# Optimization experiments

Measured on AMD Instinct MI355X. Metric: run time of the kernel, lower is better.

The kernel has to match this reference:

```python
import jax, jax.numpy as jnp
import numpy as np

B_, T_, D_MODEL = 2, 2048, 1024
EXPAND, D_STATE, D_CONV, HEADDIM = 2, 128, 4, 64
D_INNER = EXPAND * D_MODEL            # 2048
NHEADS = D_INNER // HEADDIM           # 32
CONV_DIM = D_INNER + 2 * D_STATE      # 2304 (x, B, C share the depthwise conv)
D_IN_PROJ = 2 * D_INNER + 2 * D_STATE + NHEADS  # z, xBC, dt


def _rmsnorm(x, w, eps=1e-5):
    return x * jax.lax.rsqrt(jnp.mean(x * x, axis=-1, keepdims=True) + eps) * w


def setup_inputs() -> dict:
    key = jax.random.key(0)
    ks = jax.random.split(key, 8)
    def s(k, shape, scale=0.02):
        return jax.random.normal(k, shape, jnp.float32) * scale
    x = jax.random.normal(ks[0], (B_, T_, D_MODEL), jnp.float32)
    W_in = s(ks[1], (D_MODEL, D_IN_PROJ))
    conv_w = s(ks[2], (CONV_DIM, D_CONV), 0.1)
    conv_b = jnp.zeros((CONV_DIM,), jnp.float32)
    # dt_bias = softplus^-1(dt_init) with dt in [1e-3, 1e-1], per Mamba init
    dt0 = jax.random.uniform(ks[3], (NHEADS,), minval=1e-3, maxval=1e-1)
    dt_bias = jnp.log(jnp.expm1(dt0))
    A_log = jnp.log(jax.random.uniform(ks[4], (NHEADS,), minval=1.0, maxval=16.0))
    D = jnp.ones((NHEADS,), jnp.float32)
    norm_w = jnp.ones((D_MODEL,), jnp.float32)
    gnorm_w = jnp.ones((D_INNER,), jnp.float32)
    W_out = s(ks[5], (D_INNER, D_MODEL))
    return {"x": x, "W_in": W_in, "conv_w": conv_w, "conv_b": conv_b,
            "dt_bias": dt_bias, "A_log": A_log, "D": D,
            "norm_w": norm_w, "gnorm_w": gnorm_w, "W_out": W_out}


def reference(x, W_in, conv_w, conv_b, dt_bias, A_log, D, norm_w, gnorm_w, W_out):
    res = x
    xn = _rmsnorm(x, norm_w)                       # pre-norm
    zxbcdt = xn @ W_in                             # (B,T,D_IN_PROJ)
    z = zxbcdt[..., :D_INNER]
    xBC = zxbcdt[..., D_INNER:D_INNER + CONV_DIM]
    dt = zxbcdt[..., D_INNER + CONV_DIM:]          # (B,T,H)
    # causal depthwise conv over time on concat(x,B,C)
    inp = jnp.transpose(xBC, (0, 2, 1))            # (B,C,T)
    kern = conv_w[:, None, :]                      # (C,1,K)
    conv = jax.lax.conv_general_dilated(
        inp, kern, window_strides=(1,), padding=[(D_CONV - 1, 0)],
        feature_group_count=CONV_DIM, dimension_numbers=("NCH", "OIH", "NCH"))
    xBC = jax.nn.silu(jnp.transpose(conv, (0, 2, 1)) + conv_b)
    xs = xBC[..., :D_INNER].reshape(B_, T_, NHEADS, HEADDIM)  # (B,T,H,P)
    Bm = xBC[..., D_INNER:D_INNER + D_STATE]       # (B,T,N), ngroups=1
    C = xBC[..., D_INNER + D_STATE:]               # (B,T,N)
    dt = jax.nn.softplus(dt + dt_bias)             # (B,T,H)
    A = -jnp.exp(A_log)                            # (H,)

    def step(h, inps):
        x_t, B_t, C_t, dt_t = inps                 # (B,H,P),(B,N),(B,N),(B,H)
        da = jnp.exp(dt_t * A)                     # (B,H)
        h = h * da[:, :, None, None] + (dt_t[..., None] * x_t)[..., None] * B_t[:, None, None, :]
        y = jnp.einsum("bhpn,bn->bhp", h, C_t) + D[None, :, None] * x_t
        return h, y

    h0 = jnp.zeros((B_, NHEADS, HEADDIM, D_STATE), x.dtype)
    seq = (jnp.moveaxis(xs, 1, 0), jnp.moveaxis(Bm, 1, 0),
           jnp.moveaxis(C, 1, 0), jnp.moveaxis(dt, 1, 0))
    _, ys = jax.lax.scan(step, h0, seq)            # ys: (T,B,H,P)
    y = jnp.moveaxis(ys, 0, 1).reshape(B_, T_, D_INNER)
    y = _rmsnorm(y * jax.nn.silu(z), gnorm_w)      # gated RMSNorm
    return y @ W_out + res
```

## Files before the change

kernel.cpp:

```cpp
#include <hip/hip_runtime.h>
#include <hip/hip_bf16.h>

typedef unsigned short u16;
typedef unsigned int u32;
typedef u16 u16x8 __attribute__((ext_vector_type(8)));
typedef __bf16 bf16x8 __attribute__((ext_vector_type(8)));
typedef float f32x4 __attribute__((ext_vector_type(4)));

#define B_SZ 2
#define T_SZ 2048
#define DMODEL 1024
#define DINNER 2048
#define DSTATE 128
#define NHEADS 32
#define HEADDIM 64
#define CONVDIM 2304
#define DINPROJ 4384
#define DINPROJ_P 4480
#define NROWS (B_SZ * T_SZ)
#define L_CH 128
#define NCH 16

__device__ __forceinline__ float bf2f(u16 u) {
    union { float f; u32 i; } v; v.i = ((u32)u) << 16; return v.f;
}
__device__ __forceinline__ u16 f2bf(float f) {
    union { float f; u32 i; } v; v.f = f;
    u32 r = v.i + 0x7FFFu + ((v.i >> 16) & 1u);
    return (u16)(r >> 16);
}
__device__ __forceinline__ bf16x8 ldfrag(const u16* p) {
    return __builtin_bit_cast(bf16x8, *(const u16x8*)p);
}
__device__ __forceinline__ void gload_lds16(const u16* g, u16* l) {
    __builtin_amdgcn_global_load_lds(
        (const __attribute__((address_space(1))) unsigned int*)g,
        (__attribute__((address_space(3))) unsigned int*)l, 16, 0, 0);
}

__device__ void trans_tile(const float* __restrict__ in, u16* __restrict__ out,
                           int K, int N, int n0, int k0)
{
    __shared__ u16 tile[64][66];
    const int tid = threadIdx.x;
#pragma unroll
    for (int r = 0; r < 16; r++) {
        int idx = r * 256 + tid;
        int k = idx >> 6, n = idx & 63;
        float v = (n0 + n < N) ? in[(size_t)(k0 + k) * N + n0 + n] : 0.f;
        tile[n][k] = f2bf(v);
    }
    __syncthreads();
#pragma unroll
    for (int r = 0; r < 16; r++) {
        int idx = r * 256 + tid;
        int n = idx >> 6, k = idx & 63;
        out[(size_t)(n0 + n) * K + k0 + k] = tile[n][k];
    }
}

__global__ __launch_bounds__(256) void prep_kernel(
    const float* __restrict__ W_in, u16* __restrict__ W_inT,
    const float* __restrict__ W_out, u16* __restrict__ W_outT,
    const float* __restrict__ x, const float* __restrict__ nw, u16* __restrict__ xn,
    const float* __restrict__ cw, u16* __restrict__ cwT)
{
    const int blk = blockIdx.x;
    const int tid = threadIdx.x;
    if (blk < 1120) {
        trans_tile(W_in, W_inT, DMODEL, DINPROJ, (blk % 70) * 64, (blk / 70) * 64);
    } else if (blk < 1632) {
        int idx = blk - 1120;
        trans_tile(W_out, W_outT, DINNER, DMODEL, (idx % 16) * 64, (idx / 16) * 64);
    } else if (blk < 5728) {
        const int row = blk - 1632;
        const float* xr = x + (size_t)row * DMODEL;
        float vals[4]; float ss = 0.f;
#pragma unroll
        for (int i = 0; i < 4; i++) {
            int c = tid + i * 256;
            float v = xr[c]; vals[i] = v; ss += v * v;
        }
#pragma unroll
        for (int o = 32; o; o >>= 1) ss += __shfl_xor(ss, o);
        __shared__ float red[4];
        if ((tid & 63) == 0) red[tid >> 6] = ss;
        __syncthreads();
        ss = red[0] + red[1] + red[2] + red[3];
        float sc = rsqrtf(ss / (float)DMODEL + 1e-5f);
#pragma unroll
        for (int i = 0; i < 4; i++) {
            int c = tid + i * 256;
            xn[(size_t)row * DMODEL + c] = f2bf(vals[i] * sc * nw[c]);
        }
    } else {
        for (int idx = tid; idx < 4 * CONVDIM; idx += 256) {
            int k = idx / CONVDIM, c = idx - k * CONVDIM;
            cwT[idx] = f2bf(cw[c * 4 + k]);
        }
    }
}

template<int MODE, int KC>
__global__ __launch_bounds__(256) void gemm128_kernel(
    const u16* __restrict__ A, const u16* __restrict__ BT, void* __restrict__ Cv,
    const float* __restrict__ Res, int Nst, int nbx)
{
    __shared__ u16 As[128 * 64];
    __shared__ u16 Bs[128 * 64];
    const int tid = threadIdx.x;
    const int l = tid & 63, w = tid >> 6;
    const int per = nbx * 8;
    const int grp = blockIdx.x / per, r = blockIdx.x % per;
    const int m0 = (grp * 8 + (r & 7)) * 128;
    const int n0 = (r >> 3) * 128;
    const int ml = l & 15, quad = l >> 4;
    const int wm = (w & 1) * 64, wn = (w >> 1) * 64;
    f32x4 acc[4][4] = {};
    const int srow = l >> 3;
    const int sgx = (l & 7) ^ srow;
    const u16* Ag = A + (size_t)(m0 + w * 8 + srow) * KC + sgx * 8;
    const u16* Bg = BT + (size_t)(n0 + w * 8 + srow) * KC + sgx * 8;
    u16* const As_w = &As[(w * 8) * 64];
    u16* const Bs_w = &Bs[(w * 8) * 64];

#pragma unroll 4
    for (int k0 = 0; k0 < KC; k0 += 64) {
        __syncthreads();
#pragma unroll
        for (int j = 0; j < 4; j++) {
            gload_lds16(Ag + (size_t)(j * 32) * KC + k0, As_w + j * 32 * 64);
            gload_lds16(Bg + (size_t)(j * 32) * KC + k0, Bs_w + j * 32 * 64);
        }
        __syncthreads();
#pragma unroll
        for (int ks4 = 0; ks4 < 2; ks4++) {
            bf16x8 af[4], bfr[4];
#pragma unroll
            for (int i = 0; i < 4; i++)
                af[i] = ldfrag(&As[(wm + i * 16 + ml) * 64 +
                                   (((ks4 * 4 + quad) ^ (ml & 7)) * 8)]);
#pragma unroll
            for (int i = 0; i < 4; i++)
                bfr[i] = ldfrag(&Bs[(wn + i * 16 + ml) * 64 +
                                    (((ks4 * 4 + quad) ^ (ml & 7)) * 8)]);
#pragma unroll
            for (int mt = 0; mt < 4; mt++)
#pragma unroll
                for (int nt = 0; nt < 4; nt++)
                    acc[mt][nt] = __builtin_amdgcn_mfma_f32_16x16x32_bf16(
                        af[mt], bfr[nt], acc[mt][nt], 0, 0, 0);
        }
    }
#pragma unroll
    for (int mt = 0; mt < 4; mt++)
#pragma unroll
        for (int nt = 0; nt < 4; nt++)
#pragma unroll
            for (int rg = 0; rg < 4; rg++) {
                int m = m0 + wm + mt * 16 + quad * 4 + rg;
                int n = n0 + wn + nt * 16 + ml;
                if (n < Nst) {
                    if (MODE == 0)
                        ((u16*)Cv)[(size_t)m * Nst + n] = f2bf(acc[mt][nt][rg]);
                    else
                        ((float*)Cv)[(size_t)m * Nst + n] =
                            acc[mt][nt][rg] + Res[(size_t)m * Nst + n];
                }
            }
}

template<int KC>
__global__ __launch_bounds__(256) void gemm128x64_kernel(
    const u16* __restrict__ A, const u16* __restrict__ BT, float* __restrict__ C,
    const float* __restrict__ Res, int Nst)
{
    __shared__ u16 As[128 * 64];
    __shared__ u16 Bs[64 * 64];
    const int tid = threadIdx.x;
    const int l = tid & 63, w = tid >> 6;
    const int m0 = blockIdx.y * 128;
    const int n0 = blockIdx.x * 64;
    const int ml = l & 15, quad = l >> 4;
    const int wm = w * 32;
    f32x4 acc[2][4] = {};
    const int srow = l >> 3;
    const int sgx = (l & 7) ^ srow;
    const u16* Ag = A + (size_t)(m0 + w * 8 + srow) * KC + sgx * 8;
    const u16* Bg = BT + (size_t)(n0 + w * 8 + srow) * KC + sgx * 8;
    u16* const As_w = &As[(w * 8) * 64];
    u16* const Bs_w = &Bs[(w * 8) * 64];

#pragma unroll 4
    for (int k0 = 0; k0 < KC; k0 += 64) {
        __syncthreads();
#pragma unroll
        for (int j = 0; j < 4; j++)
            gload_lds16(Ag + (size_t)(j * 32) * KC + k0, As_w + j * 32 * 64);
#pragma unroll
        for (int j = 0; j < 2; j++)
            gload_lds16(Bg + (size_t)(j * 32) * KC + k0, Bs_w + j * 32 * 64);
        __syncthreads();
#pragma unroll
        for (int ks4 = 0; ks4 < 2; ks4++) {
            bf16x8 af[2], bfr[4];
#pragma unroll
            for (int i = 0; i < 2; i++)
                af[i] = ldfrag(&As[(wm + i * 16 + ml) * 64 +
                                   (((ks4 * 4 + quad) ^ (ml & 7)) * 8)]);
#pragma unroll
            for (int i = 0; i < 4; i++)
                bfr[i] = ldfrag(&Bs[(i * 16 + ml) * 64 +
                                    (((ks4 * 4 + quad) ^ (ml & 7)) * 8)]);
#pragma unroll
            for (int mt = 0; mt < 2; mt++)
#pragma unroll
                for (int nt = 0; nt < 4; nt++)
                    acc[mt][nt] = __builtin_amdgcn_mfma_f32_16x16x32_bf16(
                        af[mt], bfr[nt], acc[mt][nt], 0, 0, 0);
        }
    }
#pragma unroll
    for (int mt = 0; mt < 2; mt++)
#pragma unroll
        for (int nt = 0; nt < 4; nt++)
#pragma unroll
            for (int rg = 0; rg < 4; rg++) {
                int m = m0 + wm + mt * 16 + quad * 4 + rg;
                int n = n0 + nt * 16 + ml;
                C[(size_t)m * Nst + n] = acc[mt][nt][rg] + Res[(size_t)m * Nst + n];
            }
}

#define NGRAN (CONVDIM / 8)
__global__ __launch_bounds__(256) void conv_silu_kernel(
    const u16* __restrict__ zx, const u16* __restrict__ cwT,
    const float* __restrict__ cb, const float* __restrict__ dt_bias,
    u16* __restrict__ out, float* __restrict__ dts)
{
    int idx = blockIdx.x * 256 + threadIdx.x;
    if (idx < B_SZ * NHEADS * T_SZ) {
        int t = idx & (T_SZ - 1);
        int bh = idx >> 11;
        int h = bh & 31, b = bh >> 5;
        float v = bf2f(zx[(size_t)(b * T_SZ + t) * DINPROJ + (DINNER + CONVDIM) + h]) + dt_bias[h];
        float sp = (v > 20.f) ? v : log1pf(expf(v));
        dts[((size_t)bh << 11) + t] = sp;
    }
    int gr = idx % NGRAN;
    int bt = idx / NGRAN;
    int t = bt & (T_SZ - 1);
    int c0 = gr * 8;
    float acc[8];
#pragma unroll
    for (int u = 0; u < 8; u++) acc[u] = cb[c0 + u];
    const u16* base = zx + (size_t)bt * DINPROJ + DINNER + c0;
#pragma unroll
    for (int k = 0; k < 4; k++) {
        int tt = t - 3 + k;
        if (tt >= 0) {
            u16x8 xv = *(const u16x8*)(base + (ptrdiff_t)(k - 3) * DINPROJ);
            u16x8 wv = *(const u16x8*)&cwT[k * CONVDIM + c0];
#pragma unroll
            for (int u = 0; u < 8; u++)
                acc[u] += bf2f(xv[u]) * bf2f(wv[u]);
        }
    }
    u16 res[8];
#pragma unroll
    for (int u = 0; u < 8; u++) {
        float s = acc[u] / (1.f + expf(-acc[u]));
        res[u] = f2bf(s);
    }
    *(u16x8*)&out[(size_t)bt * CONVDIM + c0] = *(u16x8*)res;
}

__global__ __launch_bounds__(256) void chunk_state_kernel(
    const u16* __restrict__ xbc, const float* __restrict__ dts_g,
    const float* __restrict__ A_log, float* __restrict__ cs_g, u16* __restrict__ S_bf)
{
    const int g = blockIdx.x;
    const int b = g >> 9, rem = g & 511, c = rem >> 5, h = rem & 31;
    const int tid = threadIdx.x;
    __shared__ float tmp[128], dt_l[128], d2e[128];
    __shared__ u16 Xw[64][136];
    __shared__ u16 BsT[128][136];
    const float A = -__expf(A_log[h]);
    if (tid < 128) {
        float d = dts_g[(((size_t)(b * 32 + h)) << 11) + (c << 7) + tid];
        dt_l[tid] = d; tmp[tid] = d * A;
    }
    __syncthreads();
    for (int off = 1; off < 128; off <<= 1) {
        float add = 0.f;
        if (tid < 128 && tid >= off) add = tmp[tid - off];
        __syncthreads();
        if (tid < 128) tmp[tid] += add;
        __syncthreads();
    }
    if (tid < 128) {
        float cs = tmp[tid];
        cs_g[(((size_t)(b * 32 + h)) << 11) + (c << 7) + tid] = cs;
        d2e[tid] = __expf(tmp[127] - cs) * dt_l[tid];
    }
    __syncthreads();
    const size_t rowbase = ((size_t)(b * T_SZ + c * L_CH)) * CONVDIM;
#pragma unroll
    for (int r = 0; r < 4; r++) {
        int v = tid + r * 256;
        int t = v >> 3, p0 = (v & 7) << 3;
        u16x8 xv = *(const u16x8*)&xbc[rowbase + (size_t)t * CONVDIM + h * 64 + p0];
        float s = d2e[t];
#pragma unroll
        for (int u = 0; u < 8; u++) Xw[p0 + u][t] = f2bf(bf2f(xv[u]) * s);
    }
#pragma unroll
    for (int r = 0; r < 8; r++) {
        int v = tid + r * 256;
        int t = v >> 4, n0 = (v & 15) << 3;
        u16x8 bv = *(const u16x8*)&xbc[rowbase + (size_t)t * CONVDIM + DINNER + n0];
#pragma unroll
        for (int u = 0; u < 8; u++) BsT[n0 + u][t] = bv[u];
    }
    __syncthreads();
    const int lane = tid & 63, wv = tid >> 6, ml = lane & 15, quad = lane >> 4;
    f32x4 acc[8] = {};
    for (int k0 = 0; k0 < 128; k0 += 32) {
        bf16x8 af = ldfrag(&Xw[wv * 16 + ml][k0 + quad * 8]);
#pragma unroll
        for (int nt = 0; nt < 8; nt++) {
            bf16x8 bf = ldfrag(&BsT[nt * 16 + ml][k0 + quad * 8]);
            acc[nt] = __builtin_amdgcn_mfma_f32_16x16x32_bf16(af, bf, acc[nt], 0, 0, 0);
        }
    }
    const size_t base = (size_t)g * 8192;
#pragma unroll
    for (int nt = 0; nt < 8; nt++) {
#pragma unroll
        for (int rg = 0; rg < 4; rg++) {
            int p = wv * 16 + quad * 4 + rg, n = nt * 16 + ml;
            S_bf[base + p * 128 + n] = f2bf(acc[nt][rg]);
        }
    }
}

__global__ __launch_bounds__(256) void state_pass_kernel(
    const float* __restrict__ cs_g, u16* __restrict__ S_bf)
{
    const int bh = blockIdx.x, b = bh >> 5, h = bh & 31;
    const int tid = threadIdx.x;
    float H[32];
#pragma unroll
    for (int i = 0; i < 32; i++) H[i] = 0.f;
    for (int c = 0; c < NCH; c++) {
        float decay = __expf(cs_g[(((size_t)(b * 32 + h)) << 11) + (c << 7) + 127]);
        size_t slot = ((size_t)((b * NCH + c) * 32 + h)) * 8192 + tid * 32;
        u16 tv[32];
#pragma unroll
        for (int q = 0; q < 4; q++)
            *(u16x8*)&tv[q * 8] = *(const u16x8*)&S_bf[slot + q * 8];
        u16 hw[32];
#pragma unroll
        for (int i = 0; i < 32; i++) hw[i] = f2bf(H[i]);
#pragma unroll
        for (int q = 0; q < 4; q++)
            *(u16x8*)&S_bf[slot + q * 8] = *(const u16x8*)&hw[q * 8];
#pragma unroll
        for (int i = 0; i < 32; i++) H[i] = H[i] * decay + bf2f(tv[i]);
    }
}

__global__ __launch_bounds__(256) void chunk_out_kernel(
    const u16* __restrict__ xbc, const float* __restrict__ dts_g,
    const float* __restrict__ cs_g, const u16* __restrict__ H_bf,
    const float* __restrict__ Dv, u16* __restrict__ yraw)
{
    const int g = blockIdx.x;
    const int b = g >> 9, rem = g & 511, c = rem >> 5, h = rem & 31;
    const int tid = threadIdx.x;
    __shared__ u16 Xs[64][136];
    __shared__ u16 Gs[128][40];
    __shared__ float cs_l[128], P_l[128], dt_l[128];
    const size_t rowbase = ((size_t)(b * T_SZ + c * L_CH)) * CONVDIM;
    const u16* Cg = xbc + rowbase + DINNER + 128;
    const u16* Bg = xbc + rowbase + DINNER;
    const u16* Hg = H_bf + (size_t)g * 8192;
    if (tid < 128) {
        float cs = cs_g[(((size_t)(b * 32 + h)) << 11) + (c << 7) + tid];
        cs_l[tid] = cs; P_l[tid] = __expf(cs);
        dt_l[tid] = dts_g[(((size_t)(b * 32 + h)) << 11) + (c << 7) + tid];
    }
#pragma unroll
    for (int r = 0; r < 4; r++) {
        int v = tid + r * 256; int t = v >> 3, p0 = (v & 7) << 3;
        u16x8 xv = *(const u16x8*)&xbc[rowbase + (size_t)t * CONVDIM + h * 64 + p0];
#pragma unroll
        for (int u = 0; u < 8; u++) Xs[p0 + u][t] = xv[u];
    }
    __syncthreads();
    const int lane = tid & 63, wv = tid >> 6, ml = lane & 15, quad = lane >> 4;
    const int trow = wv * 32;
    f32x4 accY[2][4] = {};
    for (int k0 = 0; k0 < 128; k0 += 32) {
        bf16x8 af0 = ldfrag(Cg + (size_t)(trow + ml) * CONVDIM + k0 + quad * 8);
        bf16x8 af1 = ldfrag(Cg + (size_t)(trow + 16 + ml) * CONVDIM + k0 + quad * 8);
#pragma unroll
        for (int pt = 0; pt < 4; pt++) {
            bf16x8 bf = ldfrag(Hg + (pt * 16 + ml) * 128 + k0 + quad * 8);
            accY[0][pt] = __builtin_amdgcn_mfma_f32_16x16x32_bf16(af0, bf, accY[0][pt], 0, 0, 0);
            accY[1][pt] = __builtin_amdgcn_mfma_f32_16x16x32_bf16(af1, bf, accY[1][pt], 0, 0, 0);
        }
    }
#pragma unroll
    for (int mt = 0; mt < 2; mt++) {
#pragma unroll
        for (int rg = 0; rg < 4; rg++) {
            float pp = P_l[trow + mt * 16 + quad * 4 + rg];
#pragma unroll
            for (int pt = 0; pt < 4; pt++) accY[mt][pt][rg] *= pp;
        }
    }
    for (int js = 0; js < 4; js++) {
        const int j0 = js * 32;
        f32x4 Ga[2][2] = {};
        for (int k0 = 0; k0 < 128; k0 += 32) {
            bf16x8 af0 = ldfrag(Cg + (size_t)(trow + ml) * CONVDIM + k0 + quad * 8);
            bf16x8 af1 = ldfrag(Cg + (size_t)(trow + 16 + ml) * CONVDIM + k0 + quad * 8);
            bf16x8 bf0 = ldfrag(Bg + (size_t)(j0 + ml) * CONVDIM + k0 + quad * 8);
            bf16x8 bf1 = ldfrag(Bg + (size_t)(j0 + 16 + ml) * CONVDIM + k0 + quad * 8);
            Ga[0][0] = __builtin_amdgcn_mfma_f32_16x16x32_bf16(af0, bf0, Ga[0][0], 0, 0, 0);
            Ga[0][1] = __builtin_amdgcn_mfma_f32_16x16x32_bf16(af0, bf1, Ga[0][1], 0, 0, 0);
            Ga[1][0] = __builtin_amdgcn_mfma_f32_16x16x32_bf16(af1, bf0, Ga[1][0], 0, 0, 0);
            Ga[1][1] = __builtin_amdgcn_mfma_f32_16x16x32_bf16(af1, bf1, Ga[1][1], 0, 0, 0);
        }
#pragma unroll
        for (int mt = 0; mt < 2; mt++) {
#pragma unroll
            for (int jt = 0; jt < 2; jt++) {
#pragma unroll
                for (int rg = 0; rg < 4; rg++) {
                    int t = trow + mt * 16 + quad * 4 + rg;
                    int j = j0 + jt * 16 + ml;
                    float val = 0.f;
                    if (t >= j) val = Ga[mt][jt][rg] * __expf(cs_l[t] - cs_l[j]) * dt_l[j];
                    Gs[t][jt * 16 + ml] = f2bf(val);
                }
            }
        }
#pragma unroll
        for (int mt = 0; mt < 2; mt++) {
            bf16x8 af = ldfrag(&Gs[trow + mt * 16 + ml][quad * 8]);
#pragma unroll
            for (int pt = 0; pt < 4; pt++) {
                bf16x8 bf = ldfrag(&Xs[pt * 16 + ml][j0 + quad * 8]);
                accY[mt][pt] = __builtin_amdgcn_mfma_f32_16x16x32_bf16(af, bf, accY[mt][pt], 0, 0, 0);
            }
        }
    }
    const float Dh = Dv[h];
    const size_t ybase = ((size_t)(b * T_SZ + c * L_CH)) * DINNER;
#pragma unroll
    for (int mt = 0; mt < 2; mt++) {
#pragma unroll
        for (int pt = 0; pt < 4; pt++) {
#pragma unroll
            for (int rg = 0; rg < 4; rg++) {
                int t = trow + mt * 16 + quad * 4 + rg;
                int p = pt * 16 + ml;
                float v = accY[mt][pt][rg] + Dh * bf2f(Xs[p][t]);
                yraw[ybase + (size_t)t * DINNER + h * 64 + p] = f2bf(v);
            }
        }
    }
}

__global__ __launch_bounds__(256) void postnorm_kernel(
    const u16* __restrict__ yraw, const u16* __restrict__ zx,
    const float* __restrict__ gw, u16* __restrict__ out)
{
    const int row = blockIdx.x;
    const u16* yr = yraw + (size_t)row * DINNER;
    const u16* zr = zx + (size_t)row * DINPROJ;
    float vals[8]; float ss = 0.f;
#pragma unroll
    for (int i = 0; i < 8; i++) {
        int c = threadIdx.x + i * 256;
        float y = bf2f(yr[c]);
        float z = bf2f(zr[c]);
        float s = z / (1.f + expf(-z));
        float t = y * s; vals[i] = t; ss += t * t;
    }
#pragma unroll
    for (int o = 32; o; o >>= 1) ss += __shfl_xor(ss, o);
    __shared__ float red[4];
    if ((threadIdx.x & 63) == 0) red[threadIdx.x >> 6] = ss;
    __syncthreads();
    ss = red[0] + red[1] + red[2] + red[3];
    float sc = rsqrtf(ss / (float)DINNER + 1e-5f);
#pragma unroll
    for (int i = 0; i < 8; i++) {
        int c = threadIdx.x + i * 256;
        out[(size_t)row * DINNER + c] = f2bf(vals[i] * sc * gw[c]);
    }
}

extern "C" void kernel_launch(void* const* d_in, const int* in_sizes, int n_in,
                              void* d_out, int out_size, void* d_ws, size_t ws_size,
                              hipStream_t stream) {
    const float* x       = (const float*)d_in[0];
    const float* W_in    = (const float*)d_in[1];
    const float* conv_w  = (const float*)d_in[2];
    const float* conv_b  = (const float*)d_in[3];
    const float* dt_bias = (const float*)d_in[4];
    const float* A_log   = (const float*)d_in[5];
    const float* Dv      = (const float*)d_in[6];
    const float* norm_w  = (const float*)d_in[7];
    const float* gnorm_w = (const float*)d_in[8];
    const float* W_out   = (const float*)d_in[9];
    float* out = (float*)d_out;

    char* ws = (char*)d_ws;
    u16*   xn    = (u16*)(ws);
    u16*   W_inT = (u16*)(ws + 8388608);
    u16*   S_bf  = (u16*)(ws);
    float* cs_g  = (float*)(ws + 16777216);
    u16*   zx    = (u16*)(ws + 17563648);
    u16*   xbc   = (u16*)(ws + 53477376);
    float* dts   = (float*)(ws + 72351744);
    u16*   yraw  = (u16*)(ws + 72876032);
    u16*   cwT   = (u16*)(ws + 89653248);
    u16*   W_outT= (u16*)(ws + 89671680);
    u16*   ynorm = yraw;

    prep_kernel<<<5729, 256, 0, stream>>>(
        W_in, W_inT, W_out, W_outT, x, norm_w, xn, conv_w, cwT);
    gemm128_kernel<0, DMODEL><<<(DINPROJ_P / 128) * (NROWS / 128), 256, 0, stream>>>(
        xn, W_inT, zx, nullptr, DINPROJ, DINPROJ_P / 128);
    conv_silu_kernel<<<(NROWS * NGRAN) / 256, 256, 0, stream>>>(
        zx, cwT, conv_b, dt_bias, xbc, dts);
    chunk_state_kernel<<<B_SZ * NCH * NHEADS, 256, 0, stream>>>(xbc, dts, A_log, cs_g, S_bf);
    state_pass_kernel<<<B_SZ * NHEADS, 256, 0, stream>>>(cs_g, S_bf);
    chunk_out_kernel<<<B_SZ * NCH * NHEADS, 256, 0, stream>>>(xbc, dts, cs_g, S_bf, Dv, yraw);
    postnorm_kernel<<<NROWS, 256, 0, stream>>>(yraw, zx, gnorm_w, ynorm);
    gemm128x64_kernel<DINNER><<<dim3(DMODEL / 64, NROWS / 128), 256, 0, stream>>>(
        ynorm, W_outT, out, x, DMODEL);
}
```

Baseline: 297.8 us.

## Pre-transpose x and B to time-major layout, drop LDS staging in SSM kernels

The conv kernel now writes x and B/C to separate buffers, and a new transpose kernel produces time-contiguous copies of x and B. The chunk_state and chunk_out kernels then read MFMA fragments straight from global memory instead of building transposed tiles in LDS. Alongside this, the chunk cumsum switches to a wavefront shuffle scan, the D skip term is folded into the diagonal of the G matrix, and state_pass prefetches the next chunk's state. The goal is to remove the strided LDS transposes and barriers, at the price of an extra kernel launch and an extra round trip of x through memory.

```diff
diff --git a/kernel.cpp b/kernel.cpp
--- a/kernel.cpp
+++ b/kernel.cpp
@@ -20,6 +20,7 @@
 #define NROWS (B_SZ * T_SZ)
 #define L_CH 128
 #define NCH 16
+#define BCW 256
 
 __device__ __forceinline__ float bf2f(u16 u) {
     union { float f; u32 i; } v; v.i = ((u32)u) << 16; return v.f;
@@ -236,7 +237,7 @@
 __global__ __launch_bounds__(256) void conv_silu_kernel(
     const u16* __restrict__ zx, const u16* __restrict__ cwT,
     const float* __restrict__ cb, const float* __restrict__ dt_bias,
-    u16* __restrict__ out, float* __restrict__ dts)
+    u16* __restrict__ Xrow, u16* __restrict__ xbcBC, float* __restrict__ dts)
 {
     int idx = blockIdx.x * 256 + threadIdx.x;
     if (idx < B_SZ * NHEADS * T_SZ) {
@@ -272,64 +273,99 @@
         float s = acc[u] / (1.f + expf(-acc[u]));
         res[u] = f2bf(s);
     }
-    *(u16x8*)&out[(size_t)bt * CONVDIM + c0] = *(u16x8*)res;
+    if (c0 < DINNER)
+        *(u16x8*)&Xrow[(size_t)bt * DINNER + c0] = *(u16x8*)res;
+    else
+        *(u16x8*)&xbcBC[(size_t)bt * BCW + (c0 - DINNER)] = *(u16x8*)res;
+}
+
+__global__ __launch_bounds__(256) void trans_xbc_kernel(
+    const u16* __restrict__ Xrow, const u16* __restrict__ xbcBC,
+    u16* __restrict__ xT, u16* __restrict__ BTg)
+{
+    __shared__ u16 tile[64][66];
+    const int blk = blockIdx.x;
+    const int tid = threadIdx.x;
+    const u16* src; u16* dst; int spitch;
+    if (blk < 2048) {
+        int b = blk >> 10, r = blk & 1023;
+        int ct = r >> 5, tt = r & 31;
+        src = Xrow + ((size_t)(b * T_SZ + tt * 64)) * DINNER + ct * 64;
+        dst = xT + ((size_t)(b * DINNER + ct * 64)) * T_SZ + tt * 64;
+        spitch = DINNER;
+    } else {
+        int idx = blk - 2048;
+        int b = idx >> 6, r = idx & 63;
+        int ct = r >> 5, tt = r & 31;
+        src = xbcBC + ((size_t)(b * T_SZ + tt * 64)) * BCW + ct * 64;
+        dst = BTg + ((size_t)(b * DSTATE + ct * 64)) * T_SZ + tt * 64;
+        spitch = BCW;
+    }
+#pragma unroll
+    for (int r = 0; r < 2; r++) {
+        int v = r * 256 + tid;
+        int i = v >> 3, j8 = (v & 7) * 8;
+        u16x8 xv = *(const u16x8*)(src + (size_t)i * spitch + j8);
+#pragma unroll
+        for (int u = 0; u < 8; u++) tile[j8 + u][i] = xv[u];
+    }
+    __syncthreads();
+#pragma unroll
+    for (int r = 0; r < 2; r++) {
+        int v = r * 256 + tid;
+        int cl = v >> 3, t8 = (v & 7) * 8;
+        u16 o[8];
+#pragma unroll
+        for (int u = 0; u < 8; u++) o[u] = tile[cl][t8 + u];
+        *(u16x8*)(dst + (size_t)cl * T_SZ + t8) = *(u16x8*)o;
+    }
 }
 
 __global__ __launch_bounds__(256) void chunk_state_kernel(
-    const u16* __restrict__ xbc, const float* __restrict__ dts_g,
-    const float* __restrict__ A_log, float* __restrict__ cs_g, u16* __restrict__ S_bf)
+    const u16* __restrict__ xT, const u16* __restrict__ BTg,
+    const float* __restrict__ dts_g, const float* __restrict__ A_log,
+    float* __restrict__ cs_g, u16* __restrict__ S_bf)
 {
     const int g = blockIdx.x;
     const int b = g >> 9, rem = g & 511, c = rem >> 5, h = rem & 31;
     const int tid = threadIdx.x;
-    __shared__ float tmp[128], dt_l[128], d2e[128];
-    __shared__ u16 Xw[64][136];
-    __shared__ u16 BsT[128][136];
+    const int lane = tid & 63;
+    __shared__ float d2e[128];
+    __shared__ float wsum[2];
     const float A = -__expf(A_log[h]);
+    float dtv = 0.f, v = 0.f;
     if (tid < 128) {
-        float d = dts_g[(((size_t)(b * 32 + h)) << 11) + (c << 7) + tid];
-        dt_l[tid] = d; tmp[tid] = d * A;
-    }
+        dtv = dts_g[(((size_t)(b * 32 + h)) << 11) + (c << 7) + tid];
+        v = dtv * A;
+    }
+#pragma unroll
+    for (int off = 1; off < 64; off <<= 1) {
+        float n = __shfl_up(v, off);
+        if (lane >= off) v += n;
+    }
+    if (tid < 128 && lane == 63) wsum[tid >> 6] = v;
     __syncthreads();
-    for (int off = 1; off < 128; off <<= 1) {
-        float add = 0.f;
-        if (tid < 128 && tid >= off) add = tmp[tid - off];
-        __syncthreads();
-        if (tid < 128) tmp[tid] += add;
-        __syncthreads();
-    }
     if (tid < 128) {
-        float cs = tmp[tid];
-        cs_g[(((size_t)(b * 32 + h)) << 11) + (c << 7) + tid] = cs;
-        d2e[tid] = __expf(tmp[127] - cs) * dt_l[tid];
+        if (tid >= 64) v += wsum[0];
+        float total = wsum[0] + wsum[1];
+        cs_g[(((size_t)(b * 32 + h)) << 11) + (c << 7) + tid] = v;
+        d2e[tid] = __expf(total - v) * dtv;
     }
     __syncthreads();
-    const size_t rowbase = ((size_t)(b * T_SZ + c * L_CH)) * CONVDIM;
-#pragma unroll
-    for (int r = 0; r < 4; r++) {
-        int v = tid + r * 256;
-        int t = v >> 3, p0 = (v & 7) << 3;
-        u16x8 xv = *(const u16x8*)&xbc[rowbase + (size_t)t * CONVDIM + h * 64 + p0];
-        float s = d2e[t];
-#pragma unroll
-        for (int u = 0; u < 8; u++) Xw[p0 + u][t] = f2bf(bf2f(xv[u]) * s);
-    }
-#pragma unroll
-    for (int r = 0; r < 8; r++) {
-        int v = tid + r * 256;
-        int t = v >> 4, n0 = (v & 15) << 3;
-        u16x8 bv = *(const u16x8*)&xbc[rowbase + (size_t)t * CONVDIM + DINNER + n0];
-#pragma unroll
-        for (int u = 0; u < 8; u++) BsT[n0 + u][t] = bv[u];
-    }
-    __syncthreads();
-    const int lane = tid & 63, wv = tid >> 6, ml = lane & 15, quad = lane >> 4;
+    const int wv = tid >> 6, ml = lane & 15, quad = lane >> 4;
+    const u16* Ag = xT + ((size_t)(b * DINNER + h * 64 + wv * 16 + ml)) * T_SZ + c * 128 + quad * 8;
+    const u16* Bg = BTg + ((size_t)(b * DSTATE + ml)) * T_SZ + c * 128 + quad * 8;
     f32x4 acc[8] = {};
     for (int k0 = 0; k0 < 128; k0 += 32) {
-        bf16x8 af = ldfrag(&Xw[wv * 16 + ml][k0 + quad * 8]);
+        u16x8 ar = *(const u16x8*)(Ag + k0);
+        u16 aw[8];
+#pragma unroll
+        for (int j = 0; j < 8; j++)
+            aw[j] = f2bf(bf2f(ar[j]) * d2e[k0 + quad * 8 + j]);
+        bf16x8 af = __builtin_bit_cast(bf16x8, *(u16x8*)aw);
 #pragma unroll
         for (int nt = 0; nt < 8; nt++) {
-            bf16x8 bf = ldfrag(&BsT[nt * 16 + ml][k0 + quad * 8]);
+            bf16x8 bf = ldfrag(Bg + (size_t)(nt * 16) * T_SZ + k0);
             acc[nt] = __builtin_amdgcn_mfma_f32_16x16x32_bf16(af, bf, acc[nt], 0, 0, 0);
         }
     }
@@ -352,13 +388,24 @@
     float H[32];
 #pragma unroll
     for (int i = 0; i < 32; i++) H[i] = 0.f;
+    u16 tvn[32], tv[32];
+    {
+        size_t slot = ((size_t)((b * NCH) * 32 + h)) * 8192 + tid * 32;
+#pragma unroll
+        for (int q = 0; q < 4; q++)
+            *(u16x8*)&tvn[q * 8] = *(const u16x8*)&S_bf[slot + q * 8];
+    }
     for (int c = 0; c < NCH; c++) {
+#pragma unroll
+        for (int i = 0; i < 32; i++) tv[i] = tvn[i];
+        if (c + 1 < NCH) {
+            size_t slotn = ((size_t)((b * NCH + c + 1) * 32 + h)) * 8192 + tid * 32;
+#pragma unroll
+            for (int q = 0; q < 4; q++)
+                *(u16x8*)&tvn[q * 8] = *(const u16x8*)&S_bf[slotn + q * 8];
+        }
         float decay = __expf(cs_g[(((size_t)(b * 32 + h)) << 11) + (c << 7) + 127]);
         size_t slot = ((size_t)((b * NCH + c) * 32 + h)) * 8192 + tid * 32;
-        u16 tv[32];
-#pragma unroll
-        for (int q = 0; q < 4; q++)
-            *(u16x8*)&tv[q * 8] = *(const u16x8*)&S_bf[slot + q * 8];
         u16 hw[32];
 #pragma unroll
         for (int i = 0; i < 32; i++) hw[i] = f2bf(H[i]);
@@ -371,39 +418,33 @@
 }
 
 __global__ __launch_bounds__(256) void chunk_out_kernel(
-    const u16* __restrict__ xbc, const float* __restrict__ dts_g,
-    const float* __restrict__ cs_g, const u16* __restrict__ H_bf,
-    const float* __restrict__ Dv, u16* __restrict__ yraw)
+    const u16* __restrict__ xbcBC, const u16* __restrict__ xT,
+    const float* __restrict__ dts_g, const float* __restrict__ cs_g,
+    const u16* __restrict__ H_bf, const float* __restrict__ Dv, u16* __restrict__ yraw)
 {
     const int g = blockIdx.x;
     const int b = g >> 9, rem = g & 511, c = rem >> 5, h = rem & 31;
     const int tid = threadIdx.x;
-    __shared__ u16 Xs[64][136];
     __shared__ u16 Gs[128][40];
     __shared__ float cs_l[128], P_l[128], dt_l[128];
-    const size_t rowbase = ((size_t)(b * T_SZ + c * L_CH)) * CONVDIM;
-    const u16* Cg = xbc + rowbase + DINNER + 128;
-    const u16* Bg = xbc + rowbase + DINNER;
+    const size_t bcbase = ((size_t)(b * T_SZ + c * L_CH)) * BCW;
+    const u16* Cg = xbcBC + bcbase + 128;
+    const u16* Bg = xbcBC + bcbase;
     const u16* Hg = H_bf + (size_t)g * 8192;
+    const u16* Xg = xT + ((size_t)(b * DINNER + h * 64)) * T_SZ + c * 128;
+    const float Dh = Dv[h];
     if (tid < 128) {
         float cs = cs_g[(((size_t)(b * 32 + h)) << 11) + (c << 7) + tid];
         cs_l[tid] = cs; P_l[tid] = __expf(cs);
         dt_l[tid] = dts_g[(((size_t)(b * 32 + h)) << 11) + (c << 7) + tid];
-    }
-#pragma unroll
-    for (int r = 0; r < 4; r++) {
-        int v = tid + r * 256; int t = v >> 3, p0 = (v & 7) << 3;
-        u16x8 xv = *(const u16x8*)&xbc[rowbase + (size_t)t * CONVDIM + h * 64 + p0];
-#pragma unroll
-        for (int u = 0; u < 8; u++) Xs[p0 + u][t] = xv[u];
     }
     __syncthreads();
     const int lane = tid & 63, wv = tid >> 6, ml = lane & 15, quad = lane >> 4;
     const int trow = wv * 32;
     f32x4 accY[2][4] = {};
     for (int k0 = 0; k0 < 128; k0 += 32) {
-        bf16x8 af0 = ldfrag(Cg + (size_t)(trow + ml) * CONVDIM + k0 + quad * 8);
-        bf16x8 af1 = ldfrag(Cg + (size_t)(trow + 16 + ml) * CONVDIM + k0 + quad * 8);
+        bf16x8 af0 = ldfrag(Cg + (size_t)(trow + ml) * BCW + k0 + quad * 8);
+        bf16x8 af1 = ldfrag(Cg + (size_t)(trow + 16 + ml) * BCW + k0 + quad * 8);
 #pragma unroll
         for (int pt = 0; pt < 4; pt++) {
             bf16x8 bf = ldfrag(Hg + (pt * 16 + ml) * 128 + k0 + quad * 8);
@@ -424,10 +465,10 @@
         const int j0 = js * 32;
         f32x4 Ga[2][2] = {};
         for (int k0 = 0; k0 < 128; k0 += 32) {
-            bf16x8 af0 = ldfrag(Cg + (size_t)(trow + ml) * CONVDIM + k0 + quad * 8);
-            bf16x8 af1 = ldfrag(Cg + (size_t)(trow + 16 + ml) * CONVDIM + k0 + quad * 8);
-            bf16x8 bf0 = ldfrag(Bg + (size_t)(j0 + ml) * CONVDIM + k0 + quad * 8);
-            bf16x8 bf1 = ldfrag(Bg + (size_t)(j0 + 16 + ml) * CONVDIM + k0 + quad * 8);
+            bf16x8 af0 = ldfrag(Cg + (size_t)(trow + ml) * BCW + k0 + quad * 8);
+            bf16x8 af1 = ldfrag(Cg + (size_t)(trow + 16 + ml) * BCW + k0 + quad * 8);
+            bf16x8 bf0 = ldfrag(Bg + (size_t)(j0 + ml) * BCW + k0 + quad * 8);
+            bf16x8 bf1 = ldfrag(Bg + (size_t)(j0 + 16 + ml) * BCW + k0 + quad * 8);
             Ga[0][0] = __builtin_amdgcn_mfma_f32_16x16x32_bf16(af0, bf0, Ga[0][0], 0, 0, 0);
             Ga[0][1] = __builtin_amdgcn_mfma_f32_16x16x32_bf16(af0, bf1, Ga[0][1], 0, 0, 0);
             Ga[1][0] = __builtin_amdgcn_mfma_f32_16x16x32_bf16(af1, bf0, Ga[1][0], 0, 0, 0);
@@ -443,6 +484,7 @@
                     int j = j0 + jt * 16 + ml;
                     float val = 0.f;
                     if (t >= j) val = Ga[mt][jt][rg] * __expf(cs_l[t] - cs_l[j]) * dt_l[j];
+                    if (t == j) val += Dh;
                     Gs[t][jt * 16 + ml] = f2bf(val);
                 }
             }
@@ -452,12 +494,11 @@
             bf16x8 af = ldfrag(&Gs[trow + mt * 16 + ml][quad * 8]);
 #pragma unroll
             for (int pt = 0; pt < 4; pt++) {
-                bf16x8 bf = ldfrag(&Xs[pt * 16 + ml][j0 + quad * 8]);
+                bf16x8 bf = ldfrag(Xg + (size_t)(pt * 16 + ml) * T_SZ + j0 + quad * 8);
                 accY[mt][pt] = __builtin_amdgcn_mfma_f32_16x16x32_bf16(af, bf, accY[mt][pt], 0, 0, 0);
             }
         }
     }
-    const float Dh = Dv[h];
     const size_t ybase = ((size_t)(b * T_SZ + c * L_CH)) * DINNER;
 #pragma unroll
     for (int mt = 0; mt < 2; mt++) {
@@ -467,8 +508,7 @@
             for (int rg = 0; rg < 4; rg++) {
                 int t = trow + mt * 16 + quad * 4 + rg;
                 int p = pt * 16 + ml;
-                float v = accY[mt][pt][rg] + Dh * bf2f(Xs[p][t]);
-                yraw[ybase + (size_t)t * DINNER + h * 64 + p] = f2bf(v);
+                yraw[ybase + (size_t)t * DINNER + h * 64 + p] = f2bf(accY[mt][pt][rg]);
             }
         }
     }
@@ -525,11 +565,14 @@
     u16*   S_bf  = (u16*)(ws);
     float* cs_g  = (float*)(ws + 16777216);
     u16*   zx    = (u16*)(ws + 17563648);
-    u16*   xbc   = (u16*)(ws + 53477376);
-    float* dts   = (float*)(ws + 72351744);
-    u16*   yraw  = (u16*)(ws + 72876032);
-    u16*   cwT   = (u16*)(ws + 89653248);
-    u16*   W_outT= (u16*)(ws + 89671680);
+    u16*   Xrow  = (u16*)(ws + 53477376);
+    u16*   yraw  = Xrow;
+    u16*   xT    = (u16*)(ws + 70254592);
+    u16*   xbcBC = (u16*)(ws + 87031808);
+    u16*   BTg   = (u16*)(ws + 89128960);
+    float* dts   = (float*)(ws + 90177536);
+    u16*   cwT   = (u16*)(ws + 90701824);
+    u16*   W_outT= (u16*)(ws + 90720256);
     u16*   ynorm = yraw;
 
     prep_kernel<<<5729, 256, 0, stream>>>(
@@ -537,10 +580,13 @@
     gemm128_kernel<0, DMODEL><<<(DINPROJ_P / 128) * (NROWS / 128), 256, 0, stream>>>(
         xn, W_inT, zx, nullptr, DINPROJ, DINPROJ_P / 128);
     conv_silu_kernel<<<(NROWS * NGRAN) / 256, 256, 0, stream>>>(
-        zx, cwT, conv_b, dt_bias, xbc, dts);
-    chunk_state_kernel<<<B_SZ * NCH * NHEADS, 256, 0, stream>>>(xbc, dts, A_log, cs_g, S_bf);
+        zx, cwT, conv_b, dt_bias, Xrow, xbcBC, dts);
+    trans_xbc_kernel<<<2176, 256, 0, stream>>>(Xrow, xbcBC, xT, BTg);
+    chunk_state_kernel<<<B_SZ * NCH * NHEADS, 256, 0, stream>>>(
+        xT, BTg, dts, A_log, cs_g, S_bf);
     state_pass_kernel<<<B_SZ * NHEADS, 256, 0, stream>>>(cs_g, S_bf);
-    chunk_out_kernel<<<B_SZ * NCH * NHEADS, 256, 0, stream>>>(xbc, dts, cs_g, S_bf, Dv, yraw);
+    chunk_out_kernel<<<B_SZ * NCH * NHEADS, 256, 0, stream>>>(
+        xbcBC, xT, dts, cs_g, S_bf, Dv, yraw);
     postnorm_kernel<<<NROWS, 256, 0, stream>>>(yraw, zx, gnorm_w, ynorm);
     gemm128x64_kernel<DINNER><<<dim3(DMODEL / 64, NROWS / 128), 256, 0, stream>>>(
         ynorm, W_outT, out, x, DMODEL);
```

Result: slower. 305.6 us (+2.6%).
